# Optimization experiments

Hardware: AMD Instinct MI355X
Metric: run time of the kernel (lower is better)

The kernel has to match this reference:

```python
import jax, jax.numpy as jnp
import numpy as np

N = 240000
B = 2
GRID = (480, 360, 32)
NUM_CLASS = 20
IGNORE_LABEL = 0
MINB = np.array([0.0, -np.pi, -4.0], np.float32)
MAXB = np.array([50.0, np.pi, 2.0], np.float32)
EPS = 1e-5


def setup_inputs() -> dict:
    key = jax.random.key(0)
    ks = jax.random.split(key, 32)
    d = {}
    d['pt_fea'] = jax.random.normal(ks[0], (N, 6), jnp.float32)
    # cylindrical coords (rho, phi, z) uniformly inside the volume
    u = jax.random.uniform(ks[1], (N, 3), jnp.float32)
    d['xyz'] = u * jnp.asarray(MAXB - MINB) + jnp.asarray(MINB)
    d['batch_idx'] = jnp.sort(jax.random.randint(ks[2], (N,), 0, B)).astype(jnp.int64)
    d['pt_lab'] = jax.random.randint(ks[3], (N,), 0, NUM_CLASS).astype(jnp.int64)
    d['shuffled_ind'] = jnp.arange(N, dtype=jnp.int64)  # identity perm (deterministic)
    i = 4
    for name, c in [('bn0', 9), ('bn1', 64), ('bn2', 128), ('bn3', 256)]:
        d[name + '_g'] = jax.random.uniform(ks[i], (c,), jnp.float32, 0.5, 1.5); i += 1
        d[name + '_b'] = jax.random.normal(ks[i], (c,), jnp.float32) * 0.1; i += 1
        d[name + '_m'] = jax.random.normal(ks[i], (c,), jnp.float32) * 0.1; i += 1
        d[name + '_v'] = jax.random.uniform(ks[i], (c,), jnp.float32, 0.5, 1.5); i += 1
    for name, (fi, fo) in [('1', (9, 64)), ('2', (64, 128)), ('3', (128, 256)), ('4', (256, 256))]:
        d['w' + name] = jax.random.normal(ks[i], (fi, fo), jnp.float32) / np.sqrt(fi); i += 1
        d['b' + name] = jax.random.normal(ks[i], (fo,), jnp.float32) * 0.01; i += 1
    d['wc'] = jax.random.normal(ks[i], (256, 16), jnp.float32) / 16.0; i += 1
    d['bc'] = jax.random.normal(ks[i], (16,), jnp.float32) * 0.01
    return d


def _bn(x, g, b, m, v):
    return (x - m) * (g * jax.lax.rsqrt(v + EPS)) + b


def _ppmodel(feat, bn0_g, bn0_b, bn0_m, bn0_v, w1, b1, bn1_g, bn1_b, bn1_m, bn1_v,
             w2, b2, bn2_g, bn2_b, bn2_m, bn2_v, w3, b3, bn3_g, bn3_b, bn3_m, bn3_v, w4, b4):
    x = _bn(feat, bn0_g, bn0_b, bn0_m, bn0_v)
    x = jax.nn.relu(_bn(x @ w1 + b1, bn1_g, bn1_b, bn1_m, bn1_v))
    x = jax.nn.relu(_bn(x @ w2 + b2, bn2_g, bn2_b, bn2_m, bn2_v))
    x = jax.nn.relu(_bn(x @ w3 + b3, bn3_g, bn3_b, bn3_m, bn3_v))
    return x @ w4 + b4  # [N, 256]


def reference(pt_fea, xyz, batch_idx, pt_lab, shuffled_ind,
              bn0_g, bn0_b, bn0_m, bn0_v, w1, b1, bn1_g, bn1_b, bn1_m, bn1_v,
              w2, b2, bn2_g, bn2_b, bn2_m, bn2_v, w3, b3, bn3_g, bn3_b, bn3_m, bn3_v,
              w4, b4, wc, bc):
    minb = jnp.asarray(MINB)
    maxb = jnp.asarray(MAXB)
    grid = jnp.asarray(np.array(GRID, np.float32))
    intervals = (maxb - minb) / (grid - 1.0)

    clamped = jnp.clip(xyz, minb, maxb)
    ind = jnp.floor((clamped - minb) / intervals).astype(jnp.int32)  # [N,3]
    voxel_centers = (ind.astype(jnp.float32) + 0.5) * intervals + minb
    rel_xyz = xyz - voxel_centers
    feat = jnp.concatenate([rel_xyz, pt_fea], axis=1)  # [N,9]

    bi = batch_idx.astype(jnp.int32)
    counts = jnp.full((B,) + GRID + (NUM_CLASS,), IGNORE_LABEL, jnp.int32)
    counts = counts.at[bi, ind[:, 0], ind[:, 1], ind[:, 2], pt_lab].add(1)
    voxel_labels = jnp.argmax(counts, axis=-1).astype(jnp.int32)  # [B,480,360,32]

    feat = feat[shuffled_ind]

    flat = ((bi.astype(jnp.int64) * GRID[0] + ind[:, 0]) * GRID[1] + ind[:, 1]) * GRID[2] + ind[:, 2]
    unq, unq_inv = jnp.unique(flat, size=N, fill_value=-1, return_inverse=True)
    unq_inv = unq_inv.reshape(-1)

    processed = _ppmodel(feat, bn0_g, bn0_b, bn0_m, bn0_v, w1, b1, bn1_g, bn1_b, bn1_m, bn1_v,
                         w2, b2, bn2_g, bn2_b, bn2_m, bn2_v, w3, b3, bn3_g, bn3_b, bn3_m, bn3_v, w4, b4)
    pooled = jax.ops.segment_max(processed, unq_inv, num_segments=N)
    seg_cnt = jax.ops.segment_sum(jnp.ones((N,), jnp.float32), unq_inv, num_segments=N)
    pooled = jnp.where(seg_cnt[:, None] > 0, pooled, 0.0)  # zero out empty (padded) segments

    processed_pooled = jax.nn.relu(pooled @ wc + bc)  # fea_compression

    cat_pt_ind = jnp.concatenate([batch_idx[:, None], ind.astype(jnp.int64)], axis=1)
    return (unq, processed_pooled, voxel_labels, cat_pt_ind)
```

## Files before the change

kernel.cpp:

```cpp
#include <hip/hip_runtime.h>
#include <stdint.h>

#define N_PTS 240000
#define NV    11059200
#define NWORDS 172800
#define NB_PT 938
#define NB_WORD 675
#define NBLK_MLP 7500
#define PA 264

typedef __bf16 bf16x8 __attribute__((ext_vector_type(8)));
typedef short  short8 __attribute__((ext_vector_type(8)));
typedef float  f32x4  __attribute__((ext_vector_type(4)));

__device__ __forceinline__ unsigned short f2bf(float f) {
  unsigned u = __builtin_bit_cast(unsigned, f);
  return (unsigned short)((u + 0x7FFFu + ((u >> 16) & 1u)) >> 16);
}
__device__ __forceinline__ float bf2f(unsigned short h) {
  unsigned u = ((unsigned)h) << 16;
  return __builtin_bit_cast(float, u);
}

__device__ __forceinline__ unsigned block_sum(unsigned v, unsigned* s4, int t) {
  #pragma unroll
  for (int o = 32; o; o >>= 1) v += __shfl_down(v, o);
  if ((t & 63) == 0) s4[t >> 6] = v;
  __syncthreads();
  unsigned r = s4[0] + s4[1] + s4[2] + s4[3];
  __syncthreads();
  return r;
}

__global__ void prep_vox_kernel(
    const float* __restrict__ bng0, const float* __restrict__ bnb0, const float* __restrict__ bnm0, const float* __restrict__ bnv0,
    const float* __restrict__ bng1, const float* __restrict__ bnb1, const float* __restrict__ bnm1, const float* __restrict__ bnv1,
    const float* __restrict__ bng2, const float* __restrict__ bnb2, const float* __restrict__ bnm2, const float* __restrict__ bnv2,
    const float* __restrict__ bng3, const float* __restrict__ bnb3, const float* __restrict__ bnm3, const float* __restrict__ bnv3,
    const float* __restrict__ w1, const float* __restrict__ b1,
    const float* __restrict__ w2, const float* __restrict__ b2,
    const float* __restrict__ w3, const float* __restrict__ b3,
    const float* __restrict__ w4, const float* __restrict__ wc,
    float* __restrict__ s0, float* __restrict__ t0, float* __restrict__ w1e, float* __restrict__ be1,
    float* __restrict__ be2, float* __restrict__ be3,
    unsigned short* __restrict__ w2t, unsigned short* __restrict__ w3t, unsigned short* __restrict__ w4t,
    unsigned short* __restrict__ wct,
    const float* __restrict__ xyz, const int* __restrict__ bidx,
    unsigned* __restrict__ flatkeys, unsigned long long* __restrict__ bitmap,
    float* __restrict__ out_cat, float* __restrict__ out_unq)
{
  if (blockIdx.x < 256) {
    const int id = blockIdx.x * 256 + threadIdx.x;
    { int c = id >> 8, k = id & 255; w4t[c * 256 + k] = f2bf(w4[k * 256 + c]); }
    if (id < 32768) { int c = id >> 7, k = id & 127;
      float s = bng3[c] * rsqrtf(bnv3[c] + 1e-5f);
      w3t[c * 128 + k] = f2bf(w3[k * 256 + c] * s); }
    if (id < 8192) { int c = id >> 6, k = id & 63;
      float s = bng2[c] * rsqrtf(bnv2[c] + 1e-5f);
      w2t[c * 64 + k] = f2bf(w2[k * 128 + c] * s); }
    if (id < 4096) { int c = id >> 8, k = id & 255;
      wct[c * 256 + k] = f2bf(wc[k * 16 + c]); }
    if (id < 576) { int k = id / 64, c = id % 64;
      float s = bng1[c] * rsqrtf(bnv1[c] + 1e-5f);
      w1e[k * 64 + c] = w1[k * 64 + c] * s; }
    if (id < 64)  { float s = bng1[id] * rsqrtf(bnv1[id] + 1e-5f); be1[id] = (b1[id] - bnm1[id]) * s + bnb1[id]; }
    if (id < 128) { float s = bng2[id] * rsqrtf(bnv2[id] + 1e-5f); be2[id] = (b2[id] - bnm2[id]) * s + bnb2[id]; }
    if (id < 256) { float s = bng3[id] * rsqrtf(bnv3[id] + 1e-5f); be3[id] = (b3[id] - bnm3[id]) * s + bnb3[id]; }
    if (id < 9)   { float s = bng0[id] * rsqrtf(bnv0[id] + 1e-5f); s0[id] = s; t0[id] = bnb0[id] - bnm0[id] * s; }
    return;
  }
  const int j = (blockIdx.x - 256) * 256 + threadIdx.x;
  if (j >= N_PTS) return;
  out_unq[j] = -1.0f;
  const float PI_F = 3.14159265358979323846f;
  const float minb[3] = {0.0f, -PI_F, -4.0f};
  const float maxb[3] = {50.0f, PI_F, 2.0f};
  const float gm1[3]  = {479.0f, 359.0f, 31.0f};
  int ind[3];
  #pragma unroll
  for (int d = 0; d < 3; ++d) {
    float itv = (maxb[d] - minb[d]) / gm1[d];
    float x  = xyz[(size_t)j * 3 + d];
    float cl = fminf(fmaxf(x, minb[d]), maxb[d]);
    ind[d] = (int)floorf((cl - minb[d]) / itv);
  }
  const int bi = bidx[j];
  const unsigned flat = ((unsigned)(bi * 480 + ind[0]) * 360u + (unsigned)ind[1]) * 32u + (unsigned)ind[2];
  flatkeys[j] = flat;
  atomicOr(&bitmap[flat >> 6], 1ull << (flat & 63u));
  float* oc = out_cat + (size_t)j * 4;
  oc[0] = (float)bi; oc[1] = (float)ind[0]; oc[2] = (float)ind[1]; oc[3] = (float)ind[2];
}

__global__ void reduce_words(const unsigned long long* __restrict__ bm, unsigned* __restrict__ bsums) {
  __shared__ unsigned sh[256];
  const int w = blockIdx.x * 256 + threadIdx.x;
  sh[threadIdx.x] = (unsigned)__popcll(bm[w]);
  __syncthreads();
  for (int s = 128; s > 0; s >>= 1) { if (threadIdx.x < s) sh[threadIdx.x] += sh[threadIdx.x + s]; __syncthreads(); }
  if (threadIdx.x == 0) bsums[blockIdx.x] = sh[0];
}

__global__ __launch_bounds__(256) void scatter_unq(
    const unsigned long long* __restrict__ bm, const unsigned* __restrict__ bsums,
    unsigned* __restrict__ wordpref, unsigned* __restrict__ unqvals, float* __restrict__ out_unq)
{
  __shared__ unsigned sh[256];
  __shared__ unsigned s4[4];
  const int t = threadIdx.x, b = blockIdx.x;
  const int w = b * 256 + t;
  unsigned long long word = bm[w];
  unsigned own = (unsigned)__popcll(word);
  sh[t] = own; __syncthreads();
  for (int off = 1; off < 256; off <<= 1) {
    unsigned v = (t >= off) ? sh[t - off] : 0u;
    __syncthreads(); sh[t] += v; __syncthreads();
  }
  unsigned v = 0;
  for (int i = t; i < b; i += 256) v += bsums[i];
  const unsigned excl = block_sum(v, s4, t);
  unsigned r = excl + sh[t] - own;
  wordpref[w] = r;
  while (word) {
    int bit = __builtin_ctzll(word);
    unsigned id = (unsigned)w * 64u + (unsigned)bit;
    unqvals[r] = id;
    out_unq[r] = (float)id;
    ++r;
    word &= word - 1;
  }
}

__global__ void inv_kernel(const unsigned* __restrict__ flatkeys, const unsigned long long* __restrict__ bm,
                           const unsigned* __restrict__ wordpref,
                           unsigned* __restrict__ unq_inv, unsigned* __restrict__ cnt) {
  const int j = blockIdx.x * 256 + threadIdx.x;
  if (j >= N_PTS) return;
  const unsigned f = flatkeys[j];
  const unsigned w = f >> 6, b = f & 63u;
  const unsigned r = wordpref[w] + (unsigned)__popcll(bm[w] & ((1ull << b) - 1ull));
  unq_inv[j] = r;
  atomicAdd(&cnt[r], 1u);
}

__global__ void reduce_cnt(const unsigned* __restrict__ cnt, unsigned* __restrict__ bsums) {
  __shared__ unsigned sh[256];
  const int j = blockIdx.x * 256 + threadIdx.x;
  sh[threadIdx.x] = (j < N_PTS) ? cnt[j] : 0u;
  __syncthreads();
  for (int s = 128; s > 0; s >>= 1) { if (threadIdx.x < s) sh[threadIdx.x] += sh[threadIdx.x + s]; __syncthreads(); }
  if (threadIdx.x == 0) bsums[blockIdx.x] = sh[0];
}

__global__ __launch_bounds__(256) void scan_cnt(
    const unsigned* __restrict__ cnt, const unsigned* __restrict__ bsums,
    unsigned* __restrict__ off, unsigned* __restrict__ cur)
{
  __shared__ unsigned sh[256];
  __shared__ unsigned s4[4];
  const int t = threadIdx.x, b = blockIdx.x;
  const int j = b * 256 + t;
  unsigned own = (j < N_PTS) ? cnt[j] : 0u;
  sh[t] = own; __syncthreads();
  for (int o = 1; o < 256; o <<= 1) {
    unsigned v = (t >= o) ? sh[t - o] : 0u;
    __syncthreads(); sh[t] += v; __syncthreads();
  }
  unsigned v = 0;
  for (int i = t; i < b; i += 256) v += bsums[i];
  const unsigned excl = block_sum(v, s4, t);
  if (j < N_PTS) { unsigned e = excl + sh[t] - own; off[j] = e; cur[j] = e; }
}

__global__ void plist_fill_kernel(const unsigned* __restrict__ unq_inv, unsigned* __restrict__ cur,
                                  unsigned long long* __restrict__ plist64,
                                  const unsigned* __restrict__ cnt, const float* __restrict__ bc,
                                  float* __restrict__ out_pooled) {
  const int j = blockIdx.x * 256 + threadIdx.x;
  if (j >= N_PTS) return;
  const unsigned r = unq_inv[j];
  plist64[atomicAdd(&cur[r], 1u)] = ((unsigned long long)r << 32) | (unsigned)j;
  if (cnt[j] == 0) {
    #pragma unroll
    for (int c = 0; c < 16; ++c) out_pooled[(size_t)j * 16 + c] = fmaxf(bc[c], 0.f);
  }
}

template<int K, int C, bool RELU, bool MIDB>
__device__ __forceinline__ void gemm_stage(
    const unsigned short* __restrict__ Wt,
    const float* __restrict__ bias,
    const unsigned short* in,
    unsigned short* outp,
    int wave, int l15, int quad)
{
  constexpr int KC = K / 32;
  constexpr int NT = C / 128;
  f32x4 acc[2][NT];
  #pragma unroll
  for (int mt = 0; mt < 2; ++mt)
    #pragma unroll
    for (int nt = 0; nt < NT; ++nt) acc[mt][nt] = (f32x4){0.f, 0.f, 0.f, 0.f};
  const unsigned short* wp[NT];
  #pragma unroll
  for (int nt = 0; nt < NT; ++nt)
    wp[nt] = Wt + (size_t)(wave * 16 * NT + nt * 16 + l15) * K + quad * 8;
  bf16x8 bcur[NT], bnxt[NT];
  #pragma unroll
  for (int nt = 0; nt < NT; ++nt)
    bcur[nt] = __builtin_bit_cast(bf16x8, *(const short8*)(wp[nt]));
  #pragma unroll
  for (int kc = 0; kc < KC; ++kc) {
    if (kc + 1 < KC) {
      #pragma unroll
      for (int nt = 0; nt < NT; ++nt)
        bnxt[nt] = __builtin_bit_cast(bf16x8, *(const short8*)(wp[nt] + (kc + 1) * 32));
    }
    #pragma unroll
    for (int mt = 0; mt < 2; ++mt) {
      bf16x8 a = __builtin_bit_cast(bf16x8, *(const short8*)&in[(mt * 16 + l15) * PA + kc * 32 + quad * 8]);
      #pragma unroll
      for (int nt = 0; nt < NT; ++nt)
        acc[mt][nt] = __builtin_amdgcn_mfma_f32_16x16x32_bf16(bcur[nt], a, acc[mt][nt], 0, 0, 0);
    }
    #pragma unroll
    for (int nt = 0; nt < NT; ++nt) bcur[nt] = bnxt[nt];
  }
  if (MIDB) __syncthreads();
  #pragma unroll
  for (int mt = 0; mt < 2; ++mt)
    #pragma unroll
    for (int nt = 0; nt < NT; ++nt) {
      const int cbase = wave * 16 * NT + nt * 16 + quad * 4;
      const f32x4 bs = *(const f32x4*)&bias[cbase];
      unsigned short h[4];
      #pragma unroll
      for (int r = 0; r < 4; ++r) {
        float y = acc[mt][nt][r] + bs[r];
        if (RELU) y = fmaxf(y, 0.f);
        h[r] = f2bf(y);
      }
      uint2 pk; pk.x = (unsigned)h[0] | ((unsigned)h[1] << 16);
      pk.y = (unsigned)h[2] | ((unsigned)h[3] << 16);
      *(uint2*)&outp[(mt * 16 + l15) * PA + cbase] = pk;
    }
  __syncthreads();
}

__global__ __launch_bounds__(512, 8) void mlp_pool_kernel(
    const float* __restrict__ ptfea, const float* __restrict__ xyz, const int* __restrict__ shuf,
    const unsigned long long* __restrict__ plist64,
    const unsigned* __restrict__ offv, const unsigned* __restrict__ cnt,
    const int* __restrict__ ptlab, const unsigned* __restrict__ unqvals,
    const float* __restrict__ s0, const float* __restrict__ t0,
    const float* __restrict__ w1e, const float* __restrict__ be1,
    const unsigned short* __restrict__ w2t, const float* __restrict__ be2,
    const unsigned short* __restrict__ w3t, const float* __restrict__ be3,
    const unsigned short* __restrict__ w4t, const float* __restrict__ b4,
    const unsigned short* __restrict__ wct, const float* __restrict__ bc,
    unsigned short* __restrict__ partials, float* __restrict__ out_pooled,
    float* __restrict__ out_lab)
{
  __shared__ __align__(16) unsigned short buf[32 * PA];
  __shared__ int segs[32];
  __shared__ int jrows[32];
  __shared__ int s_alast;
  __shared__ int s_nrun;
  __shared__ unsigned short s_runs[16];
  __shared__ unsigned char s_lead[32], s_comp[32];
  const int tid  = threadIdx.x;
  const int wave = tid >> 6, lane = tid & 63;
  const int l15 = lane & 15, quad = lane >> 4;
  const int row0 = blockIdx.x * 32;

  if (tid == 0) { s_alast = 0; s_nrun = 0; }
  if (lane < 4) {
    const int r = wave * 4 + lane;
    const unsigned long long v = plist64[row0 + r];
    jrows[r] = (int)(unsigned)v;
    segs[r]  = (int)(unsigned)(v >> 32);
  }

  {
    const int r = wave * 4 + quad, part = l15;
    const int sj = shuf[jrows[r]];
    const float PI_F = 3.14159265358979323846f;
    const float minb[3] = {0.0f, -PI_F, -4.0f};
    const float maxb[3] = {50.0f, PI_F, 2.0f};
    const float gm1[3]  = {479.0f, 359.0f, 31.0f};
    float x0[9];
    #pragma unroll
    for (int d = 0; d < 3; ++d) {
      float itv = (maxb[d] - minb[d]) / gm1[d];
      float x   = xyz[(size_t)sj * 3 + d];
      float cl  = fminf(fmaxf(x, minb[d]), maxb[d]);
      float fi  = floorf((cl - minb[d]) / itv);
      float center = (fi + 0.5f) * itv + minb[d];
      x0[d] = (x - center) * s0[d] + t0[d];
    }
    #pragma unroll
    for (int d = 0; d < 6; ++d) x0[3 + d] = ptfea[(size_t)sj * 6 + d] * s0[3 + d] + t0[3 + d];
    unsigned short h[4];
    #pragma unroll
    for (int ci = 0; ci < 4; ++ci) {
      float acc = be1[part * 4 + ci];
      #pragma unroll
      for (int k = 0; k < 9; ++k) acc += x0[k] * w1e[k * 64 + part * 4 + ci];
      h[ci] = f2bf(fmaxf(acc, 0.0f));
    }
    uint2 pk; pk.x = (unsigned)h[0] | ((unsigned)h[1] << 16);
    pk.y = (unsigned)h[2] | ((unsigned)h[3] << 16);
    *(uint2*)&buf[r * PA + part * 4] = pk;
  }
  __syncthreads();

  if (tid < 32) {
    const int r = tid;
    bool lead = (r == 0) || (segs[r] != segs[r - 1]);
    s_lead[r] = lead ? 1 : 0;
    unsigned char comp = 0;
    int e = r + 1;
    if (lead) {
      atomicMax(&s_alast, r);
      while (e < 32 && segs[e] == segs[r]) ++e;
      const unsigned s = (unsigned)segs[r];
      comp = (offv[s] == (unsigned)(row0 + r) && offv[s] + cnt[s] == (unsigned)(row0 + e)) ? 1 : 0;
    }
    s_comp[r] = comp;
    if (comp) {
      int bestl;
      if (e - r == 1) bestl = ptlab[jrows[r]];
      else {
        int bestc = 0; bestl = 32;
        for (int i = r; i < e; ++i) {
          const int li = ptlab[jrows[i]];
          int cc = 0;
          for (int k2 = r; k2 < e; ++k2) cc += (ptlab[jrows[k2]] == li) ? 1 : 0;
          if (cc > bestc || (cc == bestc && li < bestl)) { bestc = cc; bestl = li; }
        }
      }
      out_lab[unqvals[segs[r]]] = (float)bestl;
    }
    const bool multi = lead && (e - r) > 1;
    unsigned long long mm = __ballot(multi);
    if (multi) {
      int idx = (int)__popcll(mm & ((1ull << r) - 1ull));
      s_runs[idx] = (unsigned short)((r << 8) | e);
    }
    if (tid == 0) s_nrun = (int)__popcll(mm);
  }

  gemm_stage< 64, 128, true,  false>(w2t, be2, buf,       buf + 136, wave, l15, quad);
  gemm_stage<128, 256, true,  true >(w3t, be3, buf + 136, buf,       wave, l15, quad);
  gemm_stage<256, 256, false, true >(w4t, b4,  buf,       buf,       wave, l15, quad);

  if (tid < 256) {
    const int n = s_nrun;
    for (int i = 0; i < n; ++i) {
      const int re = s_runs[i];
      const int r = re >> 8, e = re & 255;
      float m = bf2f(buf[r * PA + tid]);
      for (int rr = r + 1; rr < e; ++rr) m = fmaxf(m, bf2f(buf[rr * PA + tid]));
      buf[r * PA + tid] = f2bf(m);
    }
  }
  __syncthreads();

  if (tid < 256) {
    const int c = tid;
    const int alast = s_alast;
    const size_t b2 = (size_t)blockIdx.x * 2;
    if (!s_comp[0])     partials[b2 * 256 + c]       = buf[0 * PA + c];
    if (!s_comp[alast]) partials[(b2 + 1) * 256 + c] = buf[alast * PA + c];
  }

  if (wave < 2) {
    const unsigned short* wp = wct + l15 * 256 + quad * 8;
    bf16x8 wcur = __builtin_bit_cast(bf16x8, *(const short8*)(wp));
    f32x4 acc = (f32x4){0.f, 0.f, 0.f, 0.f};
    #pragma unroll
    for (int kc = 0; kc < 8; ++kc) {
      bf16x8 wnxt;
      if (kc < 7) wnxt = __builtin_bit_cast(bf16x8, *(const short8*)(wp + (kc + 1) * 32));
      bf16x8 x = __builtin_bit_cast(bf16x8, *(const short8*)&buf[(wave * 16 + l15) * PA + kc * 32 + quad * 8]);
      acc = __builtin_amdgcn_mfma_f32_16x16x32_bf16(wcur, x, acc, 0, 0, 0);
      wcur = wnxt;
    }
    const int r1 = wave * 16 + l15;
    if (s_lead[r1] && s_comp[r1]) {
      const f32x4 bcv = *(const f32x4*)&bc[quad * 4];
      f32x4 v;
      #pragma unroll
      for (int r = 0; r < 4; ++r) v[r] = fmaxf(acc[r] + bcv[r], 0.f);
      *(f32x4*)&out_pooled[(size_t)segs[r1] * 16 + quad * 4] = v;
    }
  }
}

__global__ __launch_bounds__(256) void merge_kernel(
    const unsigned long long* __restrict__ plist64,
    const unsigned* __restrict__ offv, const unsigned* __restrict__ cnt,
    const unsigned short* __restrict__ partials,
    const int* __restrict__ ptlab, const unsigned* __restrict__ unqvals,
    const float* __restrict__ wc, const float* __restrict__ bc,
    float* __restrict__ out_pooled, float* __restrict__ out_lab)
{
  __shared__ float pooled[256];
  __shared__ float psum[256];
  const int b = blockIdx.x;
  const unsigned s = (unsigned)(plist64[(size_t)b * 32 + 31] >> 32);
  const unsigned o = offv[s], e = o + cnt[s];
  if ((o >> 5) != (unsigned)b) return;
  if (e <= (unsigned)(b + 1) * 32) return;
  const int B1 = (int)((e - 1) >> 5);
  const int c = threadIdx.x;
  float m = bf2f(partials[((size_t)2 * b + 1) * 256 + c]);
  for (int bb = b + 1; bb <= B1; ++bb)
    m = fmaxf(m, bf2f(partials[(size_t)2 * bb * 256 + c]));
  pooled[c] = m;
  __syncthreads();
  const int co = c & 15, kg = c >> 4;
  float p = 0.f;
  #pragma unroll
  for (int k = kg * 16; k < kg * 16 + 16; ++k) p += pooled[k] * wc[k * 16 + co];
  psum[c] = p;
  __syncthreads();
  if (c < 16) {
    float acc = bc[c];
    #pragma unroll
    for (int g = 0; g < 16; ++g) acc += psum[g * 16 + c];
    out_pooled[(size_t)s * 16 + c] = fmaxf(acc, 0.f);
  }
  if (c == 0) {
    int bestc = 0, bestl = 32;
    for (unsigned i = o; i < e; ++i) {
      const int li = ptlab[(unsigned)plist64[i]];
      int cc = 0;
      for (unsigned k2 = o; k2 < e; ++k2) cc += (ptlab[(unsigned)plist64[k2]] == li) ? 1 : 0;
      if (cc > bestc || (cc == bestc && li < bestl)) { bestc = cc; bestl = li; }
    }
    out_lab[unqvals[s]] = (float)bestl;
  }
}

extern "C" void kernel_launch(void* const* d_in, const int* in_sizes, int n_in,
                              void* d_out, int out_size, void* d_ws, size_t ws_size,
                              hipStream_t stream)
{
  const float* pt_fea = (const float*)d_in[0];
  const float* xyz    = (const float*)d_in[1];
  const int*   bidx   = (const int*)d_in[2];
  const int*   ptlab  = (const int*)d_in[3];
  const int*   shuf   = (const int*)d_in[4];
  const float* bng0 = (const float*)d_in[5],  *bnb0 = (const float*)d_in[6],  *bnm0 = (const float*)d_in[7],  *bnv0 = (const float*)d_in[8];
  const float* bng1 = (const float*)d_in[9],  *bnb1 = (const float*)d_in[10], *bnm1 = (const float*)d_in[11], *bnv1 = (const float*)d_in[12];
  const float* bng2 = (const float*)d_in[13], *bnb2 = (const float*)d_in[14], *bnm2 = (const float*)d_in[15], *bnv2 = (const float*)d_in[16];
  const float* bng3 = (const float*)d_in[17], *bnb3 = (const float*)d_in[18], *bnm3 = (const float*)d_in[19], *bnv3 = (const float*)d_in[20];
  const float* w1 = (const float*)d_in[21], *b1 = (const float*)d_in[22];
  const float* w2 = (const float*)d_in[23], *b2 = (const float*)d_in[24];
  const float* w3 = (const float*)d_in[25], *b3 = (const float*)d_in[26];
  const float* w4 = (const float*)d_in[27], *b4 = (const float*)d_in[28];
  const float* wc = (const float*)d_in[29], *bc = (const float*)d_in[30];

  float* out        = (float*)d_out;
  float* out_unq    = out;
  float* out_pooled = out + 240000;
  float* out_lab    = out + 4080000;
  float* out_cat    = out + 15139200;

  char* wsb = (char*)d_ws;
  size_t o = 0;
  auto alloc = [&](size_t bytes) -> void* { void* p = wsb + o; o = (o + bytes + 255) & ~(size_t)255; return p; };
  unsigned long long* bitmap = (unsigned long long*)alloc((size_t)NWORDS * 8);
  unsigned* cnt    = (unsigned*)alloc((size_t)N_PTS * 4);
  const size_t zero_bytes = o;
  float* s0  = (float*)alloc(9 * 4);
  float* t0  = (float*)alloc(9 * 4);
  float* w1e = (float*)alloc(576 * 4);
  float* be1 = (float*)alloc(64 * 4);
  float* be2 = (float*)alloc(128 * 4);
  float* be3 = (float*)alloc(256 * 4);
  unsigned short* w2t = (unsigned short*)alloc(8192 * 2);
  unsigned short* w3t = (unsigned short*)alloc(32768 * 2);
  unsigned short* w4t = (unsigned short*)alloc(65536 * 2);
  unsigned short* wct = (unsigned short*)alloc(4096 * 2);
  unsigned* flatkeys = (unsigned*)alloc((size_t)N_PTS * 4);
  unsigned* unq_inv  = (unsigned*)alloc((size_t)N_PTS * 4);
  unsigned* unqvals  = (unsigned*)alloc((size_t)N_PTS * 4);
  unsigned* offv     = (unsigned*)alloc((size_t)N_PTS * 4);
  unsigned* cur      = (unsigned*)alloc((size_t)N_PTS * 4);
  unsigned long long* plist64 = (unsigned long long*)alloc((size_t)N_PTS * 8);
  unsigned* wordpref = (unsigned*)alloc((size_t)NWORDS * 4);
  unsigned* bsumA    = (unsigned*)alloc(NB_WORD * 4);
  unsigned* bsumB    = (unsigned*)alloc(NB_PT * 4);
  unsigned short* partials = (unsigned short*)alloc((size_t)NBLK_MLP * 2 * 256 * 2);

  hipMemsetAsync(bitmap, 0, zero_bytes, stream);
  hipMemsetAsync(out_lab, 0, (size_t)NV * 4, stream);

  prep_vox_kernel<<<256 + NB_PT, 256, 0, stream>>>(
      bng0, bnb0, bnm0, bnv0, bng1, bnb1, bnm1, bnv1,
      bng2, bnb2, bnm2, bnv2, bng3, bnb3, bnm3, bnv3,
      w1, b1, w2, b2, w3, b3, w4, wc,
      s0, t0, w1e, be1, be2, be3, w2t, w3t, w4t, wct,
      xyz, bidx, flatkeys, bitmap, out_cat, out_unq);
  reduce_words<<<NB_WORD, 256, 0, stream>>>(bitmap, bsumA);
  scatter_unq<<<NB_WORD, 256, 0, stream>>>(bitmap, bsumA, wordpref, unqvals, out_unq);
  inv_kernel<<<NB_PT, 256, 0, stream>>>(flatkeys, bitmap, wordpref, unq_inv, cnt);
  reduce_cnt<<<NB_PT, 256, 0, stream>>>(cnt, bsumB);
  scan_cnt<<<NB_PT, 256, 0, stream>>>(cnt, bsumB, offv, cur);
  plist_fill_kernel<<<NB_PT, 256, 0, stream>>>(unq_inv, cur, plist64, cnt, bc, out_pooled);
  mlp_pool_kernel<<<NBLK_MLP, 512, 0, stream>>>(pt_fea, xyz, shuf, plist64, offv, cnt,
                                                ptlab, unqvals,
                                                s0, t0, w1e, be1, w2t, be2, w3t, be3, w4t, b4,
                                                wct, bc, partials, out_pooled, out_lab);
  merge_kernel<<<NBLK_MLP, 256, 0, stream>>>(plist64, offv, cnt, partials,
                                             ptlab, unqvals, wc, bc, out_pooled, out_lab);
}
```

Before: 422.8 us.

## Run MLP pooling with one wave per 32-row block and register-resident activations

Rewrites the per-block MLP so a single 64-thread wave processes each 32-point tile instead of eight waves. Activations for each GEMM stage are loaded once into registers, and output columns are produced in 64-wide chunks, using separate input and output offsets within the same shared buffer. Segment detection now uses ballots in place of shared atomics and serial scans, and it adds s_setprio around the MFMA bursts. This removes most block-wide barriers and cross-wave shared traffic, but each wave now performs eight times the MFMA work serially and holds more registers, which depends on occupancy to hide latency.

```diff
diff --git a/kernel.cpp b/kernel.cpp
--- a/kernel.cpp
+++ b/kernel.cpp
@@ -6,7 +6,7 @@
 #define NWORDS 172800
 #define NB_PT 938
 #define NB_WORD 675
-#define NBLK_MLP 7500
+#define NSEG_BLK 7500
 #define PA 264
 
 typedef __bf16 bf16x8 __attribute__((ext_vector_type(8)));
@@ -186,68 +186,65 @@
   }
 }
 
-template<int K, int C, bool RELU, bool MIDB>
-__device__ __forceinline__ void gemm_stage(
+template<int K, int C, int INO, int OUTO, bool RELU>
+__device__ __forceinline__ void stage_rs(
     const unsigned short* __restrict__ Wt,
     const float* __restrict__ bias,
-    const unsigned short* in,
-    unsigned short* outp,
-    int wave, int l15, int quad)
+    unsigned short* buf,
+    int l15, int quad)
 {
   constexpr int KC = K / 32;
-  constexpr int NT = C / 128;
-  f32x4 acc[2][NT];
+  constexpr int CP = C / 64;
+  bf16x8 areg[2][KC];
   #pragma unroll
   for (int mt = 0; mt < 2; ++mt)
     #pragma unroll
-    for (int nt = 0; nt < NT; ++nt) acc[mt][nt] = (f32x4){0.f, 0.f, 0.f, 0.f};
-  const unsigned short* wp[NT];
+    for (int kc = 0; kc < KC; ++kc)
+      areg[mt][kc] = __builtin_bit_cast(bf16x8,
+          *(const short8*)&buf[(mt * 16 + l15) * PA + INO + kc * 32 + quad * 8]);
   #pragma unroll
-  for (int nt = 0; nt < NT; ++nt)
-    wp[nt] = Wt + (size_t)(wave * 16 * NT + nt * 16 + l15) * K + quad * 8;
-  bf16x8 bcur[NT], bnxt[NT];
-  #pragma unroll
-  for (int nt = 0; nt < NT; ++nt)
-    bcur[nt] = __builtin_bit_cast(bf16x8, *(const short8*)(wp[nt]));
-  #pragma unroll
-  for (int kc = 0; kc < KC; ++kc) {
-    if (kc + 1 < KC) {
+  for (int cp = 0; cp < CP; ++cp) {
+    f32x4 acc[2][4];
+    #pragma unroll
+    for (int mt = 0; mt < 2; ++mt)
       #pragma unroll
-      for (int nt = 0; nt < NT; ++nt)
-        bnxt[nt] = __builtin_bit_cast(bf16x8, *(const short8*)(wp[nt] + (kc + 1) * 32));
-    }
-    #pragma unroll
-    for (int mt = 0; mt < 2; ++mt) {
-      bf16x8 a = __builtin_bit_cast(bf16x8, *(const short8*)&in[(mt * 16 + l15) * PA + kc * 32 + quad * 8]);
+      for (int nt = 0; nt < 4; ++nt) acc[mt][nt] = (f32x4){0.f, 0.f, 0.f, 0.f};
+    #pragma unroll
+    for (int kc = 0; kc < KC; ++kc) {
+      bf16x8 w[4];
       #pragma unroll
-      for (int nt = 0; nt < NT; ++nt)
-        acc[mt][nt] = __builtin_amdgcn_mfma_f32_16x16x32_bf16(bcur[nt], a, acc[mt][nt], 0, 0, 0);
-    }
-    #pragma unroll
-    for (int nt = 0; nt < NT; ++nt) bcur[nt] = bnxt[nt];
-  }
-  if (MIDB) __syncthreads();
-  #pragma unroll
-  for (int mt = 0; mt < 2; ++mt)
-    #pragma unroll
-    for (int nt = 0; nt < NT; ++nt) {
-      const int cbase = wave * 16 * NT + nt * 16 + quad * 4;
-      const f32x4 bs = *(const f32x4*)&bias[cbase];
-      unsigned short h[4];
+      for (int nt = 0; nt < 4; ++nt)
+        w[nt] = __builtin_bit_cast(bf16x8,
+            *(const short8*)(Wt + (size_t)(cp * 64 + nt * 16 + l15) * K + kc * 32 + quad * 8));
+      __builtin_amdgcn_s_setprio(1);
       #pragma unroll
-      for (int r = 0; r < 4; ++r) {
-        float y = acc[mt][nt][r] + bs[r];
-        if (RELU) y = fmaxf(y, 0.f);
-        h[r] = f2bf(y);
+      for (int mt = 0; mt < 2; ++mt)
+        #pragma unroll
+        for (int nt = 0; nt < 4; ++nt)
+          acc[mt][nt] = __builtin_amdgcn_mfma_f32_16x16x32_bf16(w[nt], areg[mt][kc], acc[mt][nt], 0, 0, 0);
+      __builtin_amdgcn_s_setprio(0);
+    }
+    #pragma unroll
+    for (int mt = 0; mt < 2; ++mt)
+      #pragma unroll
+      for (int nt = 0; nt < 4; ++nt) {
+        const int cbase = cp * 64 + nt * 16 + quad * 4;
+        const f32x4 bs = *(const f32x4*)&bias[cbase];
+        unsigned short h[4];
+        #pragma unroll
+        for (int r = 0; r < 4; ++r) {
+          float y = acc[mt][nt][r] + bs[r];
+          if (RELU) y = fmaxf(y, 0.f);
+          h[r] = f2bf(y);
+        }
+        uint2 pk; pk.x = (unsigned)h[0] | ((unsigned)h[1] << 16);
+        pk.y = (unsigned)h[2] | ((unsigned)h[3] << 16);
+        *(uint2*)&buf[(mt * 16 + l15) * PA + OUTO + cbase] = pk;
       }
-      uint2 pk; pk.x = (unsigned)h[0] | ((unsigned)h[1] << 16);
-      pk.y = (unsigned)h[2] | ((unsigned)h[3] << 16);
-      *(uint2*)&outp[(mt * 16 + l15) * PA + cbase] = pk;
-    }
-  __syncthreads();
-}
-
-__global__ __launch_bounds__(512, 8) void mlp_pool_kernel(
+  }
+}
+
+__global__ __launch_bounds__(64) void mlp_pool_kernel(
     const float* __restrict__ ptfea, const float* __restrict__ xyz, const int* __restrict__ shuf,
     const unsigned long long* __restrict__ plist64,
     const unsigned* __restrict__ offv, const unsigned* __restrict__ cnt,
@@ -262,28 +259,55 @@
     float* __restrict__ out_lab)
 {
   __shared__ __align__(16) unsigned short buf[32 * PA];
-  __shared__ int segs[32];
-  __shared__ int jrows[32];
-  __shared__ int s_alast;
-  __shared__ int s_nrun;
+  __shared__ int s_seg[32];
+  __shared__ int s_jr[32];
   __shared__ unsigned short s_runs[16];
   __shared__ unsigned char s_lead[32], s_comp[32];
-  const int tid  = threadIdx.x;
-  const int wave = tid >> 6, lane = tid & 63;
+  const int lane = threadIdx.x;
   const int l15 = lane & 15, quad = lane >> 4;
   const int row0 = blockIdx.x * 32;
 
-  if (tid == 0) { s_alast = 0; s_nrun = 0; }
-  if (lane < 4) {
-    const int r = wave * 4 + lane;
-    const unsigned long long v = plist64[row0 + r];
-    jrows[r] = (int)(unsigned)v;
-    segs[r]  = (int)(unsigned)(v >> 32);
-  }
+  int jr = 0, sg = 0;
+  if (lane < 32) {
+    const unsigned long long v = plist64[(size_t)row0 + lane];
+    jr = (int)(unsigned)v; sg = (int)(unsigned)(v >> 32);
+    s_jr[lane] = jr; s_seg[lane] = sg;
+  }
+  __syncthreads();
+
+  bool lead = false; int e = 0; bool comp = false;
+  if (lane < 32) lead = (lane == 0) || (sg != s_seg[lane - 1]);
+  const unsigned long long mm = __ballot(lead);
+  if (lead) {
+    unsigned long long rest = (mm | (1ull << 32)) & ~(((unsigned long long)2 << lane) - 1ull);
+    e = __builtin_ctzll(rest);
+    comp = (offv[(unsigned)sg] == (unsigned)(row0 + lane)) &&
+           (offv[(unsigned)sg] + cnt[(unsigned)sg] == (unsigned)(row0 + e));
+  }
+  if (lane < 32) { s_lead[lane] = lead ? 1 : 0; s_comp[lane] = comp ? 1 : 0; }
+  const int alast = 63 - __builtin_clzll(mm);
+  if (comp) {
+    int bestl;
+    if (e - lane == 1) bestl = ptlab[jr];
+    else {
+      int bestc = 0; bestl = 32;
+      for (int i = lane; i < e; ++i) {
+        const int li = ptlab[s_jr[i]];
+        int cc = 0;
+        for (int k2 = lane; k2 < e; ++k2) cc += (ptlab[s_jr[k2]] == li) ? 1 : 0;
+        if (cc > bestc || (cc == bestc && li < bestl)) { bestc = cc; bestl = li; }
+      }
+    }
+    out_lab[unqvals[(unsigned)sg]] = (float)bestl;
+  }
+  const bool multi = lead && (e - lane) > 1;
+  const unsigned long long mmu = __ballot(multi);
+  if (multi) s_runs[(int)__popcll(mmu & ((1ull << lane) - 1ull))] = (unsigned short)((lane << 8) | e);
+  const int nrun = (int)__popcll(mmu);
 
   {
-    const int r = wave * 4 + quad, part = l15;
-    const int sj = shuf[jrows[r]];
+    const int r = lane >> 1, part = lane & 1;
+    const int sj = shuf[s_jr[r]];
     const float PI_F = 3.14159265358979323846f;
     const float minb[3] = {0.0f, -PI_F, -4.0f};
     const float maxb[3] = {50.0f, PI_F, 2.0f};
@@ -300,99 +324,73 @@
     }
     #pragma unroll
     for (int d = 0; d < 6; ++d) x0[3 + d] = ptfea[(size_t)sj * 6 + d] * s0[3 + d] + t0[3 + d];
-    unsigned short h[4];
-    #pragma unroll
-    for (int ci = 0; ci < 4; ++ci) {
-      float acc = be1[part * 4 + ci];
+    unsigned short h[32];
+    #pragma unroll
+    for (int ci = 0; ci < 32; ++ci) {
+      float acc = be1[part * 32 + ci];
       #pragma unroll
-      for (int k = 0; k < 9; ++k) acc += x0[k] * w1e[k * 64 + part * 4 + ci];
+      for (int k = 0; k < 9; ++k) acc += x0[k] * w1e[k * 64 + part * 32 + ci];
       h[ci] = f2bf(fmaxf(acc, 0.0f));
     }
-    uint2 pk; pk.x = (unsigned)h[0] | ((unsigned)h[1] << 16);
-    pk.y = (unsigned)h[2] | ((unsigned)h[3] << 16);
-    *(uint2*)&buf[r * PA + part * 4] = pk;
-  }
-  __syncthreads();
-
-  if (tid < 32) {
-    const int r = tid;
-    bool lead = (r == 0) || (segs[r] != segs[r - 1]);
-    s_lead[r] = lead ? 1 : 0;
-    unsigned char comp = 0;
-    int e = r + 1;
-    if (lead) {
-      atomicMax(&s_alast, r);
-      while (e < 32 && segs[e] == segs[r]) ++e;
-      const unsigned s = (unsigned)segs[r];
-      comp = (offv[s] == (unsigned)(row0 + r) && offv[s] + cnt[s] == (unsigned)(row0 + e)) ? 1 : 0;
-    }
-    s_comp[r] = comp;
-    if (comp) {
-      int bestl;
-      if (e - r == 1) bestl = ptlab[jrows[r]];
-      else {
-        int bestc = 0; bestl = 32;
-        for (int i = r; i < e; ++i) {
-          const int li = ptlab[jrows[i]];
-          int cc = 0;
-          for (int k2 = r; k2 < e; ++k2) cc += (ptlab[jrows[k2]] == li) ? 1 : 0;
-          if (cc > bestc || (cc == bestc && li < bestl)) { bestc = cc; bestl = li; }
-        }
+    #pragma unroll
+    for (int i = 0; i < 4; ++i)
+      *(short8*)&buf[r * PA + part * 32 + i * 8] = *(short8*)&h[i * 8];
+  }
+  __syncthreads();
+
+  stage_rs< 64, 128,  0, 64, true >(w2t, be2, buf, l15, quad);
+  __syncthreads();
+  stage_rs<128, 256, 64,  0, true >(w3t, be3, buf, l15, quad);
+  __syncthreads();
+  stage_rs<256, 256,  0,  0, false>(w4t, b4,  buf, l15, quad);
+  __syncthreads();
+
+  for (int i = 0; i < nrun; ++i) {
+    const int re = s_runs[i];
+    const int r = re >> 8, ee = re & 255;
+    #pragma unroll
+    for (int k = 0; k < 4; ++k) {
+      const int c = lane + 64 * k;
+      float m = bf2f(buf[r * PA + c]);
+      for (int rr = r + 1; rr < ee; ++rr) m = fmaxf(m, bf2f(buf[rr * PA + c]));
+      buf[r * PA + c] = f2bf(m);
+    }
+  }
+  __syncthreads();
+
+  {
+    const size_t b2 = (size_t)blockIdx.x * 2;
+    #pragma unroll
+    for (int k = 0; k < 4; ++k) {
+      const int c = lane + 64 * k;
+      if (!s_comp[0])     partials[b2 * 256 + c]       = buf[0 * PA + c];
+      if (!s_comp[alast]) partials[(b2 + 1) * 256 + c] = buf[alast * PA + c];
+    }
+  }
+
+  {
+    const unsigned short* wp = wct + l15 * 256 + quad * 8;
+    bf16x8 wv[8];
+    #pragma unroll
+    for (int kc = 0; kc < 8; ++kc)
+      wv[kc] = __builtin_bit_cast(bf16x8, *(const short8*)(wp + kc * 32));
+    #pragma unroll
+    for (int half = 0; half < 2; ++half) {
+      f32x4 acc = (f32x4){0.f, 0.f, 0.f, 0.f};
+      #pragma unroll
+      for (int kc = 0; kc < 8; ++kc) {
+        bf16x8 x = __builtin_bit_cast(bf16x8,
+            *(const short8*)&buf[(half * 16 + l15) * PA + kc * 32 + quad * 8]);
+        acc = __builtin_amdgcn_mfma_f32_16x16x32_bf16(wv[kc], x, acc, 0, 0, 0);
       }
-      out_lab[unqvals[segs[r]]] = (float)bestl;
-    }
-    const bool multi = lead && (e - r) > 1;
-    unsigned long long mm = __ballot(multi);
-    if (multi) {
-      int idx = (int)__popcll(mm & ((1ull << r) - 1ull));
-      s_runs[idx] = (unsigned short)((r << 8) | e);
-    }
-    if (tid == 0) s_nrun = (int)__popcll(mm);
-  }
-
-  gemm_stage< 64, 128, true,  false>(w2t, be2, buf,       buf + 136, wave, l15, quad);
-  gemm_stage<128, 256, true,  true >(w3t, be3, buf + 136, buf,       wave, l15, quad);
-  gemm_stage<256, 256, false, true >(w4t, b4,  buf,       buf,       wave, l15, quad);
-
-  if (tid < 256) {
-    const int n = s_nrun;
-    for (int i = 0; i < n; ++i) {
-      const int re = s_runs[i];
-      const int r = re >> 8, e = re & 255;
-      float m = bf2f(buf[r * PA + tid]);
-      for (int rr = r + 1; rr < e; ++rr) m = fmaxf(m, bf2f(buf[rr * PA + tid]));
-      buf[r * PA + tid] = f2bf(m);
-    }
-  }
-  __syncthreads();
-
-  if (tid < 256) {
-    const int c = tid;
-    const int alast = s_alast;
-    const size_t b2 = (size_t)blockIdx.x * 2;
-    if (!s_comp[0])     partials[b2 * 256 + c]       = buf[0 * PA + c];
-    if (!s_comp[alast]) partials[(b2 + 1) * 256 + c] = buf[alast * PA + c];
-  }
-
-  if (wave < 2) {
-    const unsigned short* wp = wct + l15 * 256 + quad * 8;
-    bf16x8 wcur = __builtin_bit_cast(bf16x8, *(const short8*)(wp));
-    f32x4 acc = (f32x4){0.f, 0.f, 0.f, 0.f};
-    #pragma unroll
-    for (int kc = 0; kc < 8; ++kc) {
-      bf16x8 wnxt;
-      if (kc < 7) wnxt = __builtin_bit_cast(bf16x8, *(const short8*)(wp + (kc + 1) * 32));
-      bf16x8 x = __builtin_bit_cast(bf16x8, *(const short8*)&buf[(wave * 16 + l15) * PA + kc * 32 + quad * 8]);
-      acc = __builtin_amdgcn_mfma_f32_16x16x32_bf16(wcur, x, acc, 0, 0, 0);
-      wcur = wnxt;
-    }
-    const int r1 = wave * 16 + l15;
-    if (s_lead[r1] && s_comp[r1]) {
-      const f32x4 bcv = *(const f32x4*)&bc[quad * 4];
-      f32x4 v;
-      #pragma unroll
-      for (int r = 0; r < 4; ++r) v[r] = fmaxf(acc[r] + bcv[r], 0.f);
-      *(f32x4*)&out_pooled[(size_t)segs[r1] * 16 + quad * 4] = v;
+      const int r1 = half * 16 + l15;
+      if (s_lead[r1] && s_comp[r1]) {
+        const f32x4 bcv = *(const f32x4*)&bc[quad * 4];
+        f32x4 v;
+        #pragma unroll
+        for (int r = 0; r < 4; ++r) v[r] = fmaxf(acc[r] + bcv[r], 0.f);
+        *(f32x4*)&out_pooled[(size_t)s_seg[r1] * 16 + quad * 4] = v;
+      }
     }
   }
 }
@@ -493,7 +491,7 @@
   unsigned* wordpref = (unsigned*)alloc((size_t)NWORDS * 4);
   unsigned* bsumA    = (unsigned*)alloc(NB_WORD * 4);
   unsigned* bsumB    = (unsigned*)alloc(NB_PT * 4);
-  unsigned short* partials = (unsigned short*)alloc((size_t)NBLK_MLP * 2 * 256 * 2);
+  unsigned short* partials = (unsigned short*)alloc((size_t)NSEG_BLK * 2 * 256 * 2);
 
   hipMemsetAsync(bitmap, 0, zero_bytes, stream);
   hipMemsetAsync(out_lab, 0, (size_t)NV * 4, stream);
@@ -510,10 +508,10 @@
   reduce_cnt<<<NB_PT, 256, 0, stream>>>(cnt, bsumB);
   scan_cnt<<<NB_PT, 256, 0, stream>>>(cnt, bsumB, offv, cur);
   plist_fill_kernel<<<NB_PT, 256, 0, stream>>>(unq_inv, cur, plist64, cnt, bc, out_pooled);
-  mlp_pool_kernel<<<NBLK_MLP, 512, 0, stream>>>(pt_fea, xyz, shuf, plist64, offv, cnt,
-                                                ptlab, unqvals,
-                                                s0, t0, w1e, be1, w2t, be2, w3t, be3, w4t, b4,
-                                                wct, bc, partials, out_pooled, out_lab);
-  merge_kernel<<<NBLK_MLP, 256, 0, stream>>>(plist64, offv, cnt, partials,
+  mlp_pool_kernel<<<NSEG_BLK, 64, 0, stream>>>(pt_fea, xyz, shuf, plist64, offv, cnt,
+                                               ptlab, unqvals,
+                                               s0, t0, w1e, be1, w2t, be2, w3t, be3, w4t, b4,
+                                               wct, bc, partials, out_pooled, out_lab);
+  merge_kernel<<<NSEG_BLK, 256, 0, stream>>>(plist64, offv, cnt, partials,
                                              ptlab, unqvals, wc, bc, out_pooled, out_lab);
 }
```

After: 438.6 us. 1.04x slower.
